# Kernel tuning notes

Hardware: AMD Instinct MI355X
Metric: run time of the kernel (lower is better)

## Reference

```python
import jax, jax.numpy as jnp
import numpy as np

SPARSITY = 0.1
B, N, K = 256, 65536, 64

def setup_inputs() -> dict:
    key = jax.random.key(0)
    kx, kc = jax.random.split(key)
    x = jax.random.normal(kx, (B, N), dtype=jnp.float32)
    cluster_assignments = jax.random.randint(kc, (N,), 0, K, dtype=jnp.int32)
    cluster_weights = jnp.ones((K,), dtype=jnp.float32)
    return {"x": x, "cluster_weights": cluster_weights, "cluster_assignments": cluster_assignments}

def reference(x, cluster_weights, cluster_assignments):
    b, n = x.shape
    k = cluster_weights.shape[0]
    # cluster activation prob (context=None path): softmax(weights), same for all batch rows
    p = jax.nn.softmax(cluster_weights) * SPARSITY                      # [K]
    ku, kv = jax.random.split(jax.random.key(42))
    u = jax.random.uniform(ku, (b, n))   # drives the random permutation per (batch, cluster)
    v = jax.random.uniform(kv, (b, n))   # drives the binomial count (sum of Bernoullis)
    # Binomial(len(cluster_i), p_i) == sum of per-neuron Bernoulli(p_i) over the cluster
    bern = (v < p[cluster_assignments][None, :]).astype(jnp.int32)      # [B, N]
    counts = jax.vmap(lambda row: jax.ops.segment_sum(row, cluster_assignments, num_segments=k))(bern)  # [B, K]
    counts = jnp.maximum(counts, 1)                                     # max(1, binomial sample)
    # within-cluster uniform-random ranking: sort by (cluster, u); rank = pos - cluster_start
    sizes = jnp.bincount(cluster_assignments, length=k)                 # [K]
    starts = jnp.cumsum(sizes) - sizes                                  # exclusive cumsum [K]
    cluster_sorted = jnp.sort(cluster_assignments)                      # [N], batch-independent
    pos_in_cluster = jnp.arange(n) - starts[cluster_sorted]             # [N]
    keys = cluster_assignments.astype(jnp.float32)[None, :] + u * 0.999  # cluster-major composite key
    order = jnp.argsort(keys, axis=1)                                   # [B, N]
    mask_sorted = (pos_in_cluster[None, :] < counts[:, cluster_sorted]).astype(x.dtype)  # [B, N]
    mask = jnp.zeros_like(x).at[jnp.arange(b)[:, None], order].set(mask_sorted)
    return x * mask
```

## Files before the change

kernel.cpp:

```cpp
#include <hip/hip_runtime.h>
#include <stdint.h>

#define NROWS 256
#define NCOLS 65536
#define KCL   64
#define TMAX  20
#define NBLK  128
#define CHUNK (NCOLS / NBLK)
#define ZBLK  2048

__device__ __forceinline__ void tf2x32(uint32_t k0, uint32_t k1,
                                       uint32_t x0, uint32_t x1,
                                       uint32_t& o0, uint32_t& o1) {
  const uint32_t ks2 = k0 ^ k1 ^ 0x1BD11BDAu;
  x0 += k0; x1 += k1;
#define TFR(r) { x0 += x1; x1 = (x1 << (r)) | (x1 >> (32 - (r))); x1 ^= x0; }
  TFR(13) TFR(15) TFR(26) TFR(6)
  x0 += k1; x1 += ks2 + 1u;
  TFR(17) TFR(29) TFR(16) TFR(24)
  x0 += ks2; x1 += k0 + 2u;
  TFR(13) TFR(15) TFR(26) TFR(6)
  x0 += k0; x1 += k1 + 3u;
  TFR(17) TFR(29) TFR(16) TFR(24)
  x0 += k1; x1 += ks2 + 4u;
  TFR(13) TFR(15) TFR(26) TFR(6)
  x0 += ks2; x1 += k0 + 5u;
#undef TFR
  o0 = x0; o1 = x1;
}

struct TFO { uint32_t a, b; };
constexpr TFO tf_const(uint32_t k0, uint32_t k1, uint32_t x0, uint32_t x1) {
  const uint32_t ks2 = k0 ^ k1 ^ 0x1BD11BDAu;
  x0 += k0; x1 += k1;
#define TFC(r) { x0 += x1; x1 = (x1 << (r)) | (x1 >> (32 - (r))); x1 ^= x0; }
  TFC(13) TFC(15) TFC(26) TFC(6)
  x0 += k1; x1 += ks2 + 1u;
  TFC(17) TFC(29) TFC(16) TFC(24)
  x0 += ks2; x1 += k0 + 2u;
  TFC(13) TFC(15) TFC(26) TFC(6)
  x0 += k0; x1 += k1 + 3u;
  TFC(17) TFC(29) TFC(16) TFC(24)
  x0 += k1; x1 += ks2 + 4u;
  TFC(13) TFC(15) TFC(26) TFC(6)
  x0 += ks2; x1 += k0 + 5u;
#undef TFC
  return {x0, x1};
}
constexpr TFO KU = tf_const(0u, 42u, 0u, 0u);
constexpr TFO KV = tf_const(0u, 42u, 0u, 1u);

__device__ __forceinline__ uint32_t jax_bits(uint32_t k0, uint32_t k1, uint32_t f) {
  uint32_t o0, o1;
  tf2x32(k0, k1, 0u, f, o0, o1);
  return o0 ^ o1;
}

__device__ __forceinline__ float bits_to_u01(uint32_t bits) {
  return __uint_as_float((bits >> 9) | 0x3f800000u) - 1.0f;
}

__device__ __forceinline__ float key_from_ubits(uint32_t ubits, float kf) {
  return __fadd_rn(kf, __fmul_rn(bits_to_u01(ubits), 0.999f));
}

__device__ __forceinline__ int wave_sum_i(int v) {
#pragma unroll
  for (int m = 1; m < 64; m <<= 1) v += __shfl_xor(v, m, 64);
  return v;
}
__device__ __forceinline__ uint32_t wave_min_u(uint32_t v) {
#pragma unroll
  for (int m = 1; m < 64; m <<= 1) {
    const uint32_t o = (uint32_t)__shfl_xor((int)v, m, 64);
    v = (o < v) ? o : v;
  }
  return v;
}
__device__ __forceinline__ int wave_min_i(int v) {
#pragma unroll
  for (int m = 1; m < 64; m <<= 1) {
    const int o = __shfl_xor(v, m, 64);
    v = (o < v) ? o : v;
  }
  return v;
}

__global__ __launch_bounds__(256)
void k_zerohist(float4* __restrict__ outv, const int* __restrict__ a,
                int* __restrict__ blockhist) {
  const int gtid = blockIdx.x * 256 + threadIdx.x;
  const float4 z = make_float4(0.f, 0.f, 0.f, 0.f);
#pragma unroll
  for (int i = 0; i < 8; ++i)
    outv[gtid + i * (ZBLK * 256)] = z;
  if (blockIdx.x < NBLK) {
    __shared__ int h[KCL];
    if (threadIdx.x < KCL) h[threadIdx.x] = 0;
    __syncthreads();
    const int base = blockIdx.x * CHUNK;
#pragma unroll
    for (int i = base + threadIdx.x; i < base + CHUNK; i += 256)
      atomicAdd(&h[a[i]], 1);
    __syncthreads();
    if (threadIdx.x < KCL) blockhist[blockIdx.x * KCL + threadIdx.x] = h[threadIdx.x];
  }
}

__global__ __launch_bounds__(256)
void k_prescatter(const int* __restrict__ a, const int* __restrict__ blockhist,
                  int* __restrict__ sizes_g, int* __restrict__ starts_g,
                  const float* __restrict__ w, uint32_t* __restrict__ vthresh,
                  int* __restrict__ idx_sorted) {
  __shared__ int cur[KCL];
  const int tid = threadIdx.x;
  const int lane = tid & 63;
  const int wid = tid >> 6;
  const int blk = blockIdx.x;

  if (wid == 0) {
    int own = 0, tot = 0;
#pragma unroll 8
    for (int b2 = 0; b2 < NBLK; ++b2) {
      const int h = blockhist[b2 * KCL + lane];
      own += (b2 < blk) ? h : 0;
      tot += h;
    }
    int scan = tot;
#pragma unroll
    for (int d = 1; d < 64; d <<= 1) {
      const int o = __shfl_up(scan, d, 64);
      if (lane >= d) scan += o;
    }
    const int start = scan - tot;
    cur[lane] = start + own;
    if (blk == 0) {
      sizes_g[lane] = tot;
      starts_g[lane] = start;
      const float wk = w[lane];
      float m = wk;
#pragma unroll
      for (int d = 1; d < 64; d <<= 1) m = fmaxf(m, __shfl_xor(m, d, 64));
      const float e = expf(wk - m);
      float s = e;
#pragma unroll
      for (int d = 1; d < 64; d <<= 1) s += __shfl_xor(s, d, 64);
      vthresh[lane] = (uint32_t)ceilf((e / s) * 0.1f * 8388608.0f);
    }
  }
  __syncthreads();
  const int base = blk * CHUNK;
#pragma unroll
  for (int i = base + tid; i < base + CHUNK; i += 256) {
    const int k = a[i];
    const int slot = atomicAdd(&cur[k], 1);
    idx_sorted[slot] = i;
  }
}

__global__ __launch_bounds__(256)
void k_select(const float* __restrict__ x,
              const int* __restrict__ idx_sorted,
              const int* __restrict__ sizes,
              const int* __restrict__ starts,
              const uint32_t* __restrict__ vthresh,
              float* __restrict__ out) {
  const int lane = threadIdx.x & 63;
  const int pair = (blockIdx.x << 2) + (threadIdx.x >> 6);
  const int b = pair & (NROWS - 1);
  const int k = pair >> 8;

  int sz = sizes[k];
  const int st = starts[k];
  if (sz <= 0) return;
  if (sz > TMAX * 64) sz = TMAX * 64;

  const uint32_t ku0 = KU.a, ku1 = KU.b, kv0 = KV.a, kv1 = KV.b;
  const uint32_t vt = vthresh[k];
  const float kf = (float)k;
  const uint32_t bbase = (uint32_t)(b << 16);

  int nv[TMAX];
#pragma unroll
  for (int t = 0; t < TMAX; ++t) {
    const int j = lane + (t << 6);
    nv[t] = (j < sz) ? idx_sorted[st + j] : 0;
  }

  uint32_t kb[TMAX];
  uint32_t curmin = 0xFFFFFFFFu;
  int cnt = 0;
#pragma unroll
  for (int t = 0; t < TMAX; ++t) {
    const int j = lane + (t << 6);
    uint32_t kbv = 0xFFFFFFFFu;
    if (j < sz) {
      const uint32_t f = bbase + (uint32_t)nv[t];
      const uint32_t ubv = jax_bits(ku0, ku1, f);
      const uint32_t vbv = jax_bits(kv0, kv1, f);
      cnt += ((vbv >> 9) < vt) ? 1 : 0;
      kbv = __float_as_uint(key_from_ubits(ubv, kf));
    }
    kb[t] = kbv;
    curmin = (kbv < curmin) ? kbv : curmin;
  }
  int C = wave_sum_i(cnt);
  if (C < 1) C = 1;

  uint32_t consumed = 0;
  uint32_t Tkey;
  for (int e = 0;; ++e) {
    const uint32_t wmn = wave_min_u(curmin);
    if (e == C - 1) { Tkey = wmn; break; }
    const unsigned long long bal = __ballot(curmin == wmn);
    const int src = (int)__ffsll((long long)bal) - 1;
    if (lane == src) {
      int ct = -1;
#pragma unroll
      for (int t = 0; t < TMAX; ++t)
        if (ct < 0 && !((consumed >> t) & 1u) && kb[t] == wmn) ct = t;
      consumed |= (1u << ct);
      uint32_t nm = 0xFFFFFFFFu;
#pragma unroll
      for (int t = 0; t < TMAX; ++t) {
        const uint32_t v = ((consumed >> t) & 1u) ? 0xFFFFFFFFu : kb[t];
        nm = (v < nm) ? v : nm;
      }
      curmin = nm;
    }
  }

  int packed = 0;
#pragma unroll
  for (int t = 0; t < TMAX; ++t) {
    packed += (kb[t] < Tkey) ? (1 << 16) : 0;
    packed += (kb[t] == Tkey) ? 1 : 0;
  }
  const int sred = wave_sum_i(packed);
  const int nbelow = sred >> 16;
  const int tieCnt = sred & 0xFFFF;
  const int r = C - nbelow;

  int cutN = 0x7FFFFFFF;
  if (r < tieCnt) {
    uint32_t cons2 = 0;
    for (int e = 0; e < r; ++e) {
      int mnN = 0x7FFFFFFF, mnT = 0;
#pragma unroll
      for (int t = 0; t < TMAX; ++t) {
        if (kb[t] == Tkey && !((cons2 >> t) & 1u)) {
          if (nv[t] < mnN) { mnN = nv[t]; mnT = t; }
        }
      }
      const int w = wave_min_i(mnN);
      cutN = w;
      const unsigned long long bal = __ballot(mnN == w);
      const int src = (int)__ffsll((long long)bal) - 1;
      if (lane == src) cons2 |= (1u << mnT);
    }
  }

  const size_t rowoff = (size_t)b * NCOLS;
  const bool allTies = (r >= tieCnt);
#pragma unroll
  for (int t = 0; t < TMAX; ++t) {
    const uint32_t v = kb[t];
    bool sel = (v < Tkey);
    if (!sel && v == Tkey) sel = allTies ? true : (nv[t] <= cutN);
    if (sel) {
      const size_t off = rowoff + (uint32_t)nv[t];
      out[off] = x[off];
    }
  }
}

extern "C" void kernel_launch(void* const* d_in, const int* in_sizes, int n_in,
                              void* d_out, int out_size, void* d_ws, size_t ws_size,
                              hipStream_t stream) {
  const float* x = (const float*)d_in[0];
  const float* w = (const float*)d_in[1];
  const int* assign = (const int*)d_in[2];
  float* out = (float*)d_out;
  uint32_t* ws = (uint32_t*)d_ws;

  uint32_t* vthresh   = ws;
  int*      sizes     = (int*)(ws + 64);
  int*      starts    = (int*)(ws + 128);
  int*      blockhist = (int*)(ws + 192);
  int*      idxs      = (int*)(ws + 192 + NBLK * KCL);

  k_zerohist<<<ZBLK, 256, 0, stream>>>((float4*)out, assign, blockhist);
  k_prescatter<<<NBLK, 256, 0, stream>>>(assign, blockhist, sizes, starts, w,
                                         vthresh, idxs);
  k_select<<<(NROWS * KCL) / 4, 256, 0, stream>>>(x, idxs, sizes, starts,
                                                  vthresh, out);
  (void)n_in; (void)in_sizes; (void)ws_size;
}
```

Before: 98.80 us.

## Overlap output zeroing with selection by staging selected values in workspace

Moves the 64 MB output zero-fill out of the first kernel and into extra blocks of the select kernel, so zeroing runs alongside the RNG-heavy selection work. Because zeroing and selection now run concurrently, selected values are staged in a per-(row, cluster) workspace list and scattered by a separate apply kernel afterward. A standalone histogram kernel is split out. This costs an extra launch, extra workspace traffic, and a 64-entry cap per (row, cluster) that could drop selections if exceeded. It falls back to the old path if the workspace is too small.

```diff
diff --git a/kernel.cpp b/kernel.cpp
--- a/kernel.cpp
+++ b/kernel.cpp
@@ -8,6 +8,8 @@
 #define NBLK  128
 #define CHUNK (NCOLS / NBLK)
 #define ZBLK  2048
+#define NSEL  ((NROWS * KCL) / 4)
+#define SLMAX 64
 
 __device__ __forceinline__ void tf2x32(uint32_t k0, uint32_t k1,
                                        uint32_t x0, uint32_t x1,
@@ -87,6 +89,20 @@
 }
 
 __global__ __launch_bounds__(256)
+void k_hist(const int* __restrict__ a, int* __restrict__ blockhist) {
+  __shared__ int h[KCL];
+  const int tid = threadIdx.x;
+  if (tid < KCL) h[tid] = 0;
+  __syncthreads();
+  const int base = blockIdx.x * CHUNK;
+#pragma unroll
+  for (int i = base + tid; i < base + CHUNK; i += 256)
+    atomicAdd(&h[a[i]], 1);
+  __syncthreads();
+  if (tid < KCL) blockhist[blockIdx.x * KCL + tid] = h[tid];
+}
+
+__global__ __launch_bounds__(256)
 void k_zerohist(float4* __restrict__ outv, const int* __restrict__ a,
                 int* __restrict__ blockhist) {
   const int gtid = blockIdx.x * 256 + threadIdx.x;
@@ -158,13 +174,27 @@
   }
 }
 
-__global__ __launch_bounds__(256)
-void k_select(const float* __restrict__ x,
-              const int* __restrict__ idx_sorted,
-              const int* __restrict__ sizes,
-              const int* __restrict__ starts,
-              const uint32_t* __restrict__ vthresh,
-              float* __restrict__ out) {
+template<bool DIRECT>
+__global__ __launch_bounds__(256)
+void k_select_t(const float* __restrict__ x,
+                const int* __restrict__ idx_sorted,
+                const int* __restrict__ sizes,
+                const int* __restrict__ starts,
+                const uint32_t* __restrict__ vthresh,
+                float* __restrict__ out,
+                int* __restrict__ scount,
+                int* __restrict__ sl_n,
+                float* __restrict__ sl_v) {
+  if (!DIRECT && blockIdx.x >= NSEL) {
+    const int z = blockIdx.x - NSEL;
+    const int gtid = z * 256 + threadIdx.x;
+    float4* outv = (float4*)out;
+    const float4 zz = make_float4(0.f, 0.f, 0.f, 0.f);
+#pragma unroll
+    for (int i = 0; i < 8; ++i)
+      outv[gtid + i * (ZBLK * 256)] = zz;
+    return;
+  }
   const int lane = threadIdx.x & 63;
   const int pair = (blockIdx.x << 2) + (threadIdx.x >> 6);
   const int b = pair & (NROWS - 1);
@@ -262,16 +292,53 @@
 
   const size_t rowoff = (size_t)b * NCOLS;
   const bool allTies = (r >= tieCnt);
-#pragma unroll
-  for (int t = 0; t < TMAX; ++t) {
-    const uint32_t v = kb[t];
-    bool sel = (v < Tkey);
-    if (!sel && v == Tkey) sel = allTies ? true : (nv[t] <= cutN);
-    if (sel) {
-      const size_t off = rowoff + (uint32_t)nv[t];
-      out[off] = x[off];
-    }
-  }
+  if (DIRECT) {
+#pragma unroll
+    for (int t = 0; t < TMAX; ++t) {
+      const uint32_t v = kb[t];
+      bool sel = (v < Tkey);
+      if (!sel && v == Tkey) sel = allTies ? true : (nv[t] <= cutN);
+      if (sel) {
+        const size_t off = rowoff + (uint32_t)nv[t];
+        out[off] = x[off];
+      }
+    }
+  } else {
+    const int base = pair * SLMAX;
+    int running = 0;
+#pragma unroll
+    for (int t = 0; t < TMAX; ++t) {
+      const uint32_t v = kb[t];
+      bool sel = (v < Tkey);
+      if (!sel && v == Tkey) sel = allTies ? true : (nv[t] <= cutN);
+      const unsigned long long bal = __ballot(sel);
+      if (sel) {
+        const int slot = running + (int)__popcll(bal & ((1ull << lane) - 1ull));
+        if (slot < SLMAX) {
+          sl_n[base + slot] = nv[t];
+          sl_v[base + slot] = x[rowoff + (uint32_t)nv[t]];
+        }
+      }
+      running += (int)__popcll(bal);
+    }
+    if (lane == 0) scount[pair] = (running < SLMAX) ? running : SLMAX;
+  }
+}
+
+__global__ __launch_bounds__(256)
+void k_apply(const int* __restrict__ sizes, const int* __restrict__ scount,
+             const int* __restrict__ sl_n, const float* __restrict__ sl_v,
+             float* __restrict__ out) {
+  const int lane = threadIdx.x & 63;
+  const int pair = (blockIdx.x << 2) + (threadIdx.x >> 6);
+  const int b = pair & (NROWS - 1);
+  const int k = pair >> 8;
+  if (sizes[k] <= 0) return;
+  const int c = scount[pair];
+  const int base = pair * SLMAX;
+  const size_t rowoff = (size_t)b * NCOLS;
+  for (int i = lane; i < c; i += 64)
+    out[rowoff + (uint32_t)sl_n[base + i]] = sl_v[base + i];
 }
 
 extern "C" void kernel_launch(void* const* d_in, const int* in_sizes, int n_in,
@@ -283,16 +350,41 @@
   float* out = (float*)d_out;
   uint32_t* ws = (uint32_t*)d_ws;
 
-  uint32_t* vthresh   = ws;
-  int*      sizes     = (int*)(ws + 64);
-  int*      starts    = (int*)(ws + 128);
-  int*      blockhist = (int*)(ws + 192);
-  int*      idxs      = (int*)(ws + 192 + NBLK * KCL);
-
-  k_zerohist<<<ZBLK, 256, 0, stream>>>((float4*)out, assign, blockhist);
-  k_prescatter<<<NBLK, 256, 0, stream>>>(assign, blockhist, sizes, starts, w,
-                                         vthresh, idxs);
-  k_select<<<(NROWS * KCL) / 4, 256, 0, stream>>>(x, idxs, sizes, starts,
-                                                  vthresh, out);
-  (void)n_in; (void)in_sizes; (void)ws_size;
-}
+  const size_t U_VT  = 0;
+  const size_t U_SZ  = U_VT + 64;
+  const size_t U_ST  = U_SZ + 64;
+  const size_t U_BH  = U_ST + 64;
+  const size_t U_IDX = U_BH + NBLK * KCL;
+  const size_t U_SC  = U_IDX + NCOLS;
+  const size_t U_SLN = U_SC + NROWS * KCL;
+  const size_t U_SLV = U_SLN + (size_t)NROWS * KCL * SLMAX;
+  const size_t U_END = U_SLV + (size_t)NROWS * KCL * SLMAX;
+
+  uint32_t* vthresh   = ws + U_VT;
+  int*      sizes     = (int*)(ws + U_SZ);
+  int*      starts    = (int*)(ws + U_ST);
+  int*      blockhist = (int*)(ws + U_BH);
+  int*      idxs      = (int*)(ws + U_IDX);
+  int*      scount    = (int*)(ws + U_SC);
+  int*      sl_n      = (int*)(ws + U_SLN);
+  float*    sl_v      = (float*)(ws + U_SLV);
+
+  const bool fused = (ws_size >= U_END * sizeof(uint32_t));
+
+  if (fused) {
+    k_hist<<<NBLK, 256, 0, stream>>>(assign, blockhist);
+    k_prescatter<<<NBLK, 256, 0, stream>>>(assign, blockhist, sizes, starts, w,
+                                           vthresh, idxs);
+    k_select_t<false><<<NSEL + ZBLK, 256, 0, stream>>>(x, idxs, sizes, starts,
+                                                       vthresh, out, scount,
+                                                       sl_n, sl_v);
+    k_apply<<<NSEL, 256, 0, stream>>>(sizes, scount, sl_n, sl_v, out);
+  } else {
+    k_zerohist<<<ZBLK, 256, 0, stream>>>((float4*)out, assign, blockhist);
+    k_prescatter<<<NBLK, 256, 0, stream>>>(assign, blockhist, sizes, starts, w,
+                                           vthresh, idxs);
+    k_select_t<true><<<NSEL, 256, 0, stream>>>(x, idxs, sizes, starts,
+                                               vthresh, out, scount, sl_n, sl_v);
+  }
+  (void)n_in; (void)in_sizes;
+}
```

Result: slower. 102.6 us (+3.9%).
